# Optimization experiments

Measured on AMD Instinct MI355X. Metric: run time of the kernel, lower is better.

Reference implementation:

```python
import math
import jax, jax.numpy as jnp
import numpy as np

N_HEAD = 8
BLOCK_SIZE = 1024
LN_EPS = 1e-5


def _layer_norm(x, g, b):
    mu = jnp.mean(x, axis=-1, keepdims=True)
    var = jnp.var(x, axis=-1, keepdims=True)
    return (x - mu) * jax.lax.rsqrt(var + LN_EPS) * g + b


def _skew(QEr):
    # QEr: (B, nh, L, L) -> pad one zero column on the left, reshape, drop first row
    B, nh, nr, nc = QEr.shape
    padded = jnp.pad(QEr, ((0, 0), (0, 0), (0, 0), (1, 0)))  # (B, nh, nr, nc+1)
    reshaped = padded.reshape(B, nh, nc + 1, nr)
    return reshaped[:, :, 1:, :]  # (B, nh, nr, nc)


def _attn(x, W_qkv, b_qkv, W_o, b_o, Er):
    B, L, D = x.shape
    hs = D // N_HEAD
    qkv = x @ W_qkv + b_qkv  # (B, L, 3D)
    q, k, v = jnp.split(qkv, 3, axis=-1)
    # (B, nh, L, hs)
    q = q.reshape(B, L, N_HEAD, hs).transpose(0, 2, 1, 3)
    k = k.reshape(B, L, N_HEAD, hs).transpose(0, 2, 1, 3)
    v = v.reshape(B, L, N_HEAD, hs).transpose(0, 2, 1, 3)
    start = BLOCK_SIZE - L
    Er_t = Er[start:, :].T  # (hs, L)
    QEr = q @ Er_t  # (B, nh, L, L)
    Srel = _skew(QEr)
    scores = (jnp.einsum('bhqd,bhkd->bhqk', q, k) + Srel) * (1.0 / math.sqrt(hs))
    causal = jnp.tril(jnp.ones((L, L), dtype=bool))
    scores = jnp.where(causal, scores, jnp.float32(-jnp.inf))
    att = jax.nn.softmax(scores, axis=-1)
    y = jnp.einsum('bhqk,bhkd->bhqd', att, v)
    y = y.transpose(0, 2, 1, 3).reshape(B, L, D)
    return y @ W_o + b_o


def reference(x, W_qkv, b_qkv, W_o, b_o, Er, ln1_g, ln1_b, ln2_g, ln2_b,
              W_fc, b_fc, W_proj, b_proj):
    x = x + _attn(_layer_norm(x, ln1_g, ln1_b), W_qkv, b_qkv, W_o, b_o, Er)
    h = _layer_norm(x, ln2_g, ln2_b) @ W_fc + b_fc
    h = jax.nn.gelu(h, approximate=False)
    h = h @ W_proj + b_proj
    return x + h


def setup_inputs() -> dict:
    key = jax.random.key(0)
    ks = jax.random.split(key, 8)
    B, L, D, F = 8, 1024, 1024, 4096
    hs = D // N_HEAD
    s = lambda fan_in: 1.0 / math.sqrt(fan_in)
    return {
        'x': jax.random.normal(ks[0], (B, L, D), dtype=jnp.float32),
        'W_qkv': jax.random.normal(ks[1], (D, 3 * D), dtype=jnp.float32) * s(D),
        'b_qkv': jnp.zeros((3 * D,), dtype=jnp.float32),
        'W_o': jax.random.normal(ks[2], (D, D), dtype=jnp.float32) * s(D),
        'b_o': jnp.zeros((D,), dtype=jnp.float32),
        'Er': jax.random.normal(ks[3], (BLOCK_SIZE, hs), dtype=jnp.float32),
        'ln1_g': jnp.ones((D,), dtype=jnp.float32),
        'ln1_b': jnp.zeros((D,), dtype=jnp.float32),
        'ln2_g': jnp.ones((D,), dtype=jnp.float32),
        'ln2_b': jnp.zeros((D,), dtype=jnp.float32),
        'W_fc': jax.random.normal(ks[4], (D, F), dtype=jnp.float32) * s(D),
        'b_fc': jnp.zeros((F,), dtype=jnp.float32),
        'W_proj': jax.random.normal(ks[5], (F, D), dtype=jnp.float32) * s(F),
        'b_proj': jnp.zeros((D,), dtype=jnp.float32),
    }
```

## Files before the change

### kernel.cpp

```cpp
#include <hip/hip_runtime.h>
#include <hip/hip_bf16.h>
#include <math.h>

#define BB 8
#define LL 1024
#define DD 1024
#define FF 4096
#define NHH 8
#define HSS 128
#define SCALE 0.08838834764831845f
#define TRI(qi, kt) ((qi) * ((qi) + 1) / 2 + (kt))

typedef __bf16 bf16;
typedef __bf16 bf16x8 __attribute__((ext_vector_type(8)));
typedef float f32x4 __attribute__((ext_vector_type(4)));
typedef _Float16 f16;
typedef _Float16 f16x4 __attribute__((ext_vector_type(4)));

__device__ inline void async_copy16(const void* g, void* l) {
  __builtin_amdgcn_global_load_lds(
      (const __attribute__((address_space(1))) unsigned int*)g,
      (__attribute__((address_space(3))) unsigned int*)l, 16, 0, 0);
}

#define FENCE() asm volatile("" ::: "memory")
#define BARRIER() do { FENCE(); __builtin_amdgcn_s_barrier(); FENCE(); } while (0)
#define VMCNT6() asm volatile("s_waitcnt vmcnt(6)" ::: "memory")

__global__ __launch_bounds__(256)
void transpose_cast_kernel(const float* __restrict__ W, bf16* __restrict__ Wt,
                           int K, int N) {
  __shared__ float tile[32][33];
  int n0 = blockIdx.x * 32, k0 = blockIdx.y * 32;
  int tx = threadIdx.x, ty = threadIdx.y;
#pragma unroll
  for (int i = 0; i < 32; i += 8)
    tile[ty + i][tx] = W[(size_t)(k0 + ty + i) * N + n0 + tx];
  __syncthreads();
#pragma unroll
  for (int i = 0; i < 32; i += 8)
    Wt[(size_t)(n0 + ty + i) * K + k0 + tx] = (bf16)tile[tx][ty + i];
}

__global__ __launch_bounds__(256)
void pack_er_kernel(const float* __restrict__ Er, bf16* __restrict__ ErP) {
  int g = blockIdx.x, tid = threadIdx.x;
  int l15 = tid & 15, quad = (tid >> 4) & 3, st = tid >> 6;
  const float* src = Er + (size_t)(g * 16 + l15) * HSS + st * 32 + quad * 8;
  bf16* dst = ErP + (size_t)g * 2048 + tid * 8;
#pragma unroll
  for (int j = 0; j < 8; j++) dst[j] = (bf16)src[j];
}

__global__ __launch_bounds__(256)
void ln_kernel(const float* __restrict__ x, const float* __restrict__ g,
               const float* __restrict__ bta, bf16* __restrict__ out) {
  int row = blockIdx.x;
  int tid = threadIdx.x;
  const float4 v = ((const float4*)(x + (size_t)row * DD))[tid];
  float s = v.x + v.y + v.z + v.w;
  float s2 = v.x * v.x + v.y * v.y + v.z * v.z + v.w * v.w;
#pragma unroll
  for (int o = 32; o > 0; o >>= 1) {
    s += __shfl_down(s, o);
    s2 += __shfl_down(s2, o);
  }
  __shared__ float a1[4], a2[4];
  int wave = tid >> 6;
  if ((tid & 63) == 0) { a1[wave] = s; a2[wave] = s2; }
  __syncthreads();
  s = a1[0] + a1[1] + a1[2] + a1[3];
  s2 = a2[0] + a2[1] + a2[2] + a2[3];
  float mu = s * (1.0f / DD);
  float rstd = rsqrtf(s2 * (1.0f / DD) - mu * mu + 1e-5f);
  float4 gv = ((const float4*)g)[tid];
  float4 bv = ((const float4*)bta)[tid];
  bf16* o4 = out + (size_t)row * DD + tid * 4;
  o4[0] = (bf16)((v.x - mu) * rstd * gv.x + bv.x);
  o4[1] = (bf16)((v.y - mu) * rstd * gv.y + bv.y);
  o4[2] = (bf16)((v.z - mu) * rstd * gv.z + bv.z);
  o4[3] = (bf16)((v.w - mu) * rstd * gv.w + bv.w);
}

template <int EPI>
__global__ __launch_bounds__(512)
void gemm256_kernel(const bf16* __restrict__ A, const bf16* __restrict__ Bt,
                    const float* __restrict__ bias, void* __restrict__ Cout,
                    int M, int N, int K) {
  __shared__ bf16 Als[2][256 * 64];
  __shared__ bf16 Bls[2][256 * 64];
  int tid = threadIdx.x;
  int wave = tid >> 6, lane = tid & 63;
  int l15 = lane & 15, quad = lane >> 4;
  int wmi = wave >> 2, wni = wave & 3;
  int m0 = blockIdx.y * 256, n0 = blockIdx.x * 256;

  int u0 = tid, u1 = tid + 512;
  int r0 = u0 >> 3, c0 = ((u0 & 7) ^ (r0 & 7)) << 3;
  int r1 = u1 >> 3, c1 = ((u1 & 7) ^ (r1 & 7)) << 3;
  const bf16* aB0 = A + (size_t)(m0 + r0) * K + c0;
  const bf16* aB1 = A + (size_t)(m0 + r1) * K + c1;
  const bf16* bB0 = Bt + (size_t)(n0 + r0) * K + c0;
  const bf16* bB1 = Bt + (size_t)(n0 + r1) * K + c1;
  int d0 = u0 * 8, d1 = u1 * 8;

  auto stageA = [&](int b, int h, int t) {
    size_t off = (size_t)h * 128 * K + (size_t)t * 64;
    async_copy16(aB0 + off, &Als[b][h * 8192 + d0]);
    async_copy16(aB1 + off, &Als[b][h * 8192 + d1]);
  };
  auto stageB = [&](int b, int h, int t) {
    size_t off = (size_t)h * 128 * K + (size_t)t * 64;
    async_copy16(bB0 + off, &Bls[b][h * 8192 + d0]);
    async_copy16(bB1 + off, &Bls[b][h * 8192 + d1]);
  };

  f32x4 acc[8][4] = {};
  bf16x8 af[2][4], bfr[2][2];

  auto readA = [&](int b, int qm) {
#pragma unroll
    for (int kk = 0; kk < 2; kk++)
#pragma unroll
      for (int mt = 0; mt < 4; mt++) {
        int ra = qm * 128 + wmi * 64 + mt * 16 + l15;
        af[kk][mt] = *(const bf16x8*)&Als[b][ra * 64 + (((kk * 4 + quad) ^ (ra & 7)) << 3)];
      }
  };
  auto readB = [&](int b, int qn) {
#pragma unroll
    for (int kk = 0; kk < 2; kk++)
#pragma unroll
      for (int nt = 0; nt < 2; nt++) {
        int rb = qn * 128 + wni * 32 + nt * 16 + l15;
        bfr[kk][nt] = *(const bf16x8*)&Bls[b][rb * 64 + (((kk * 4 + quad) ^ (rb & 7)) << 3)];
      }
  };
  auto mfma16 = [&](int qm, int qn) {
    __builtin_amdgcn_s_setprio(1);
#pragma unroll
    for (int kk = 0; kk < 2; kk++)
#pragma unroll
      for (int mt = 0; mt < 4; mt++)
#pragma unroll
        for (int nt = 0; nt < 2; nt++)
          acc[qm * 4 + mt][qn * 2 + nt] = __builtin_amdgcn_mfma_f32_16x16x32_bf16(
              af[kk][mt], bfr[kk][nt], acc[qm * 4 + mt][qn * 2 + nt], 0, 0, 0);
    __builtin_amdgcn_s_setprio(0);
  };

  int nk = K >> 6;
  stageA(0, 0, 0); stageB(0, 0, 0); stageB(0, 1, 0); stageA(0, 1, 0);
  stageA(1, 0, 1); stageB(1, 1, 1);
  VMCNT6();
  BARRIER();

  for (int t = 0; t < nk; t++) {
    int cur = t & 1;
    readA(cur, 0); readB(cur, 0);
    if (t + 1 < nk) stageB(cur ^ 1, 0, t + 1);
    BARRIER();
    mfma16(0, 0);
    BARRIER();
    readB(cur, 1);
    if (t + 1 < nk) stageA(cur ^ 1, 1, t + 1);
    VMCNT6();
    BARRIER();
    mfma16(0, 1);
    BARRIER();
    readA(cur, 1);
    if (t + 2 < nk) stageA(cur, 0, t + 2);
    BARRIER();
    mfma16(1, 1);
    BARRIER();
    readB(cur, 0);
    if (t + 2 < nk) stageB(cur, 1, t + 2);
    VMCNT6();
    BARRIER();
    mfma16(1, 0);
    BARRIER();
  }

#pragma unroll
  for (int MT = 0; MT < 8; MT++) {
#pragma unroll
    for (int NT = 0; NT < 4; NT++) {
      int col = n0 + (NT >> 1) * 128 + wni * 32 + (NT & 1) * 16 + l15;
      float bv = bias[col];
#pragma unroll
      for (int r = 0; r < 4; r++) {
        int row = m0 + (MT >> 2) * 128 + wmi * 64 + (MT & 3) * 16 + quad * 4 + r;
        float v = acc[MT][NT][r] + bv;
        if (EPI == 1) v = 0.5f * v * (1.0f + erff(v * 0.7071067811865475f));
        ((bf16*)Cout)[(size_t)row * N + col] = (bf16)v;
      }
    }
  }
}

template <int EPI>
__global__ __launch_bounds__(256)
void gemm_kernel(const bf16* __restrict__ A, const bf16* __restrict__ Bt,
                 const float* __restrict__ bias, const float* __restrict__ res,
                 void* __restrict__ Cout, int M, int N, int K) {
  __shared__ bf16 Als[128 * 64];
  __shared__ bf16 Bls[128 * 64];
  int tid = threadIdx.x;
  int wave = tid >> 6, lane = tid & 63;
  int l15 = lane & 15, quad = lane >> 4;

  int m0 = blockIdx.y * 128, n0 = blockIdx.x * 128;
  int wm = (wave >> 1) * 64, wn = (wave & 1) * 64;
  f32x4 acc[4][4] = {};

  const bf16* asrc[4];
  const bf16* bsrc[4];
  int ldso[4];
#pragma unroll
  for (int i = 0; i < 4; i++) {
    int u = i * 256 + tid;
    int row = u >> 3, c = u & 7;
    int g = c ^ (row & 7);
    asrc[i] = A + (size_t)(m0 + row) * K + g * 8;
    bsrc[i] = Bt + (size_t)(n0 + row) * K + g * 8;
    ldso[i] = u * 8;
  }

  for (int k0 = 0; k0 < K; k0 += 64) {
    __syncthreads();
#pragma unroll
    for (int i = 0; i < 4; i++) {
      async_copy16(asrc[i] + k0, &Als[ldso[i]]);
      async_copy16(bsrc[i] + k0, &Bls[ldso[i]]);
    }
    __syncthreads();

    bf16x8 af[2][4], bfr[2][4];
#pragma unroll
    for (int kk = 0; kk < 2; kk++) {
#pragma unroll
      for (int mt = 0; mt < 4; mt++) {
        int ra = wm + mt * 16 + l15;
        af[kk][mt] = *(const bf16x8*)&Als[ra * 64 + (((kk * 4 + quad) ^ (ra & 7)) << 3)];
        int rb = wn + mt * 16 + l15;
        bfr[kk][mt] = *(const bf16x8*)&Bls[rb * 64 + (((kk * 4 + quad) ^ (rb & 7)) << 3)];
      }
    }
#pragma unroll
    for (int kk = 0; kk < 2; kk++)
#pragma unroll
      for (int mt = 0; mt < 4; mt++)
#pragma unroll
        for (int nt = 0; nt < 4; nt++)
          acc[mt][nt] = __builtin_amdgcn_mfma_f32_16x16x32_bf16(af[kk][mt], bfr[kk][nt],
                                                                acc[mt][nt], 0, 0, 0);
  }

#pragma unroll
  for (int mt = 0; mt < 4; mt++) {
#pragma unroll
    for (int nt = 0; nt < 4; nt++) {
      int col = n0 + wn + nt * 16 + l15;
      float bv = bias[col];
#pragma unroll
      for (int r = 0; r < 4; r++) {
        int row = m0 + wm + mt * 16 + quad * 4 + r;
        float v = acc[mt][nt][r] + bv;
        if (EPI == 1) v = 0.5f * v * (1.0f + erff(v * 0.7071067811865475f));
        if (EPI == 2) {
          v += res[(size_t)row * N + col];
          ((float*)Cout)[(size_t)row * N + col] = v;
        } else {
          ((bf16*)Cout)[(size_t)row * N + col] = (bf16)v;
        }
      }
    }
  }
}

__global__ __launch_bounds__(256)
void pack_kv_kernel(const bf16* __restrict__ qkv, bf16* __restrict__ Kpack,
                    bf16* __restrict__ Vpack) {
  __shared__ bf16 Vst[64][132];
  int kt = blockIdx.x, h = blockIdx.y, b = blockIdx.z;
  int tid = threadIdx.x;
  const size_t rs = 3 * DD;
  const bf16* kb = qkv + (size_t)b * LL * rs + (size_t)(kt * 64) * rs + DD + h * HSS;
  const bf16* vb = kb + DD;
  bf16* kp = Kpack + ((size_t)(b * NHH + h) * 16 + kt) * (64 * 128);
  bf16* vp = Vpack + ((size_t)(b * NHH + h) * 16 + kt) * (128 * 64);
#pragma unroll
  for (int i = 0; i < 4; i++) {
    int u = i * 256 + tid;
    int kk = u >> 4, c = u & 15;
    bf16x8 kv = *(const bf16x8*)(kb + (size_t)kk * rs + c * 8);
    *(bf16x8*)(kp + kk * 128 + ((c ^ kk) & 15) * 8) = kv;
    *(bf16x8*)&Vst[kk][c * 8] = *(const bf16x8*)(vb + (size_t)kk * rs + c * 8);
  }
  __syncthreads();
#pragma unroll
  for (int i = 0; i < 4; i++) {
    int u = i * 256 + tid;
    int d = u >> 3, c = u & 7;
    bf16x8 t;
#pragma unroll
    for (int j = 0; j < 8; j++) t[j] = Vst[c * 8 + j][d];
    *(bf16x8*)(vp + d * 64 + ((c ^ (d & 7))) * 8) = t;
  }
}

__global__ __launch_bounds__(256)
void relband_kernel(const bf16* __restrict__ qkv, const bf16* __restrict__ ErP,
                    f16* __restrict__ band) {
  int tid = threadIdx.x, wave = tid >> 6, lane = tid & 63;
  int l15 = lane & 15, quad = lane >> 4;
  int h = blockIdx.y, b = blockIdx.z;
  const size_t rs = 3 * DD;
  const bf16* qbase = qkv + (size_t)b * LL * rs + h * HSS;
  f16* bbase = band + (size_t)(b * NHH + h) * (136 * 4096);

#pragma unroll 1
  for (int ph = 0; ph < 2; ph++) {
    int qb = ph ? 15 - blockIdx.x : blockIdx.x;
    int qw0 = qb * 64 + wave * 16;

    bf16x8 qf[4];
#pragma unroll
    for (int st = 0; st < 4; st++)
      qf[st] = *(const bf16x8*)(qbase + (size_t)(qw0 + l15) * rs + st * 32 + quad * 8);

#pragma unroll 1
    for (int kt = 0; kt <= qb; kt++) {
      int k0 = kt * 64;
      int kmax_off = qw0 + 15 - k0;
      int m_base = 1008 - qw0 + k0;
      int gb = m_base >> 4;
      int ntR = (kmax_off >> 4) + 1;
      if (ntR > 4) ntR = 4;

      f32x4 rr[5] = {};
#pragma unroll
      for (int n = 0; n < 5; n++) {
        if (n <= ntR) {
          int g = gb + n;
          if (g > 63) g = 63;
          const bf16* ep = ErP + (size_t)g * 2048 + lane * 8;
#pragma unroll
          for (int st = 0; st < 4; st++) {
            bf16x8 ef = *(const bf16x8*)(ep + st * 512);
            rr[n] = __builtin_amdgcn_mfma_f32_16x16x32_bf16(qf[st], ef, rr[n], 0, 0, 0);
          }
        }
      }

      f16x4 sf[4];
#pragma unroll
      for (int rg = 0; rg < 4; rg++) {
        int qloc = quad * 4 + rg;
        int tt = 15 - qloc + l15;
        int src = (lane & 48) | (tt & 15);
        float shv[5];
#pragma unroll
        for (int n = 0; n < 5; n++)
          shv[n] = (n <= ntR) ? __shfl(rr[n][rg], src) : 0.f;
#pragma unroll
        for (int nt = 0; nt < 4; nt++)
          sf[nt][rg] = (f16)((tt & 16) ? shv[nt + 1] : shv[nt]);
      }
      f16* tb = bbase + (size_t)TRI(qb, kt) * 4096;
#pragma unroll
      for (int nt = 0; nt < 4; nt++)
        if (nt * 16 <= kmax_off)
          *(f16x4*)(tb + (wave * 4 + nt) * 256 + l15 * 16 + quad * 4) = sf[nt];
    }
  }
}

__global__ __launch_bounds__(256)
void flash_kernel(const bf16* __restrict__ qkv, const bf16* __restrict__ Kpack,
                  const bf16* __restrict__ Vpack, const f16* __restrict__ band,
                  bf16* __restrict__ y) {
  __shared__ bf16 Kls[2][64 * 128];
  __shared__ bf16 Vls[2][128 * 64];
  __shared__ bf16 Pls[4][16][72];

  int tid = threadIdx.x, wave = tid >> 6, lane = tid & 63;
  int l15 = lane & 15, quad = lane >> 4;
  int h = blockIdx.y, b = blockIdx.z;

  const size_t rs = 3 * DD;
  const bf16* qbase = qkv + (size_t)b * LL * rs + h * HSS;
  const bf16* kp = Kpack + (size_t)(b * NHH + h) * 16 * (64 * 128);
  const bf16* vp = Vpack + (size_t)(b * NHH + h) * 16 * (128 * 64);
  const f16* bnd = band + (size_t)(b * NHH + h) * (136 * 4096);

  int buf = 0;
#pragma unroll 1
  for (int ph = 0; ph < 2; ph++) {
    int qb = ph ? 15 - blockIdx.x : blockIdx.x;
    int qw0 = qb * 64 + wave * 16;
    int nkt = qb + 1;

    bf16x8 qf[4];
#pragma unroll
    for (int st = 0; st < 4; st++)
      qf[st] = *(const bf16x8*)(qbase + (size_t)(qw0 + l15) * rs + st * 32 + quad * 8);

    {
      const bf16* ks = kp;
      const bf16* vs = vp;
#pragma unroll
      for (int i = 0; i < 4; i++) {
        int off = (wave * 4 + i) * 512 + lane * 8;
        async_copy16(ks + off, &Kls[buf][off]);
        async_copy16(vs + off, &Vls[buf][off]);
      }
    }

    f32x4 o[8] = {};
    float mrow[4] = {-INFINITY, -INFINITY, -INFINITY, -INFINITY};
    float lrow[4] = {0.f, 0.f, 0.f, 0.f};

#pragma unroll 1
    for (int kt = 0; kt < nkt; kt++) {
      int k0 = kt * 64;
      int kmax_off = qw0 + 15 - k0;
      __syncthreads();

      const f16* tb = bnd + (size_t)TRI(qb, kt) * 4096;
      f16x4 srl[4] = {};
#pragma unroll
      for (int nt = 0; nt < 4; nt++)
        if (nt * 16 <= kmax_off)
          srl[nt] = *(const f16x4*)(tb + (wave * 4 + nt) * 256 + l15 * 16 + quad * 4);

      if (kt + 1 < nkt) {
        const bf16* ks = kp + (size_t)(kt + 1) * (64 * 128);
        const bf16* vs = vp + (size_t)(kt + 1) * (128 * 64);
#pragma unroll
        for (int i = 0; i < 4; i++) {
          int off = (wave * 4 + i) * 512 + lane * 8;
          async_copy16(ks + off, &Kls[buf ^ 1][off]);
          async_copy16(vs + off, &Vls[buf ^ 1][off]);
        }
      }

      f32x4 sa[4] = {};
#pragma unroll
      for (int nt = 0; nt < 4; nt++) {
        if (nt * 16 <= kmax_off) {
          int kk = nt * 16 + l15;
#pragma unroll
          for (int st = 0; st < 4; st++) {
            bf16x8 kf = *(const bf16x8*)&Kls[buf][kk * 128 + (((st * 4 + quad) ^ l15) & 15) * 8];
            sa[nt] = __builtin_amdgcn_mfma_f32_16x16x32_bf16(qf[st], kf, sa[nt], 0, 0, 0);
          }
        }
      }

      float pmx[4] = {-INFINITY, -INFINITY, -INFINITY, -INFINITY};
#pragma unroll
      for (int nt = 0; nt < 4; nt++) {
        if (nt * 16 <= kmax_off) {
          int kg = k0 + nt * 16 + l15;
#pragma unroll
          for (int rg = 0; rg < 4; rg++) {
            int qg = qw0 + quad * 4 + rg;
            float v = (sa[nt][rg] + (float)srl[nt][rg]) * SCALE;
            v = (kg <= qg) ? v : -INFINITY;
            sa[nt][rg] = v;
            pmx[rg] = fmaxf(pmx[rg], v);
          }
        } else {
#pragma unroll
          for (int rg = 0; rg < 4; rg++) sa[nt][rg] = -INFINITY;
        }
      }

#pragma unroll
      for (int rg = 0; rg < 4; rg++) {
        float v = pmx[rg];
        v = fmaxf(v, __shfl_xor(v, 1));
        v = fmaxf(v, __shfl_xor(v, 2));
        v = fmaxf(v, __shfl_xor(v, 4));
        v = fmaxf(v, __shfl_xor(v, 8));
        float mnew = fmaxf(mrow[rg], v);
        float alpha = __expf(mrow[rg] - mnew);
        mrow[rg] = mnew;
        lrow[rg] *= alpha;
#pragma unroll
        for (int nt = 0; nt < 8; nt++) o[nt][rg] *= alpha;
        pmx[rg] = mnew;
      }
      float ls[4] = {0.f, 0.f, 0.f, 0.f};
#pragma unroll
      for (int nt = 0; nt < 4; nt++)
#pragma unroll
        for (int rg = 0; rg < 4; rg++) {
          float p = __expf(sa[nt][rg] - pmx[rg]);
          ls[rg] += p;
          Pls[wave][quad * 4 + rg][nt * 16 + l15] = (bf16)p;
        }
#pragma unroll
      for (int rg = 0; rg < 4; rg++) {
        float v = ls[rg];
        v += __shfl_xor(v, 1);
        v += __shfl_xor(v, 2);
        v += __shfl_xor(v, 4);
        v += __shfl_xor(v, 8);
        lrow[rg] += v;
      }

      bf16x8 pf[2];
#pragma unroll
      for (int s2 = 0; s2 < 2; s2++)
        pf[s2] = *(const bf16x8*)&Pls[wave][l15][s2 * 32 + quad * 8];
#pragma unroll
      for (int nt = 0; nt < 8; nt++) {
        int d = nt * 16 + l15;
#pragma unroll
        for (int s2 = 0; s2 < 2; s2++) {
          if (s2 * 32 <= kmax_off) {
            bf16x8 vf = *(const bf16x8*)&Vls[buf][d * 64 + (((s2 * 4 + quad) ^ (l15 & 7)) & 7) * 8];
            o[nt] = __builtin_amdgcn_mfma_f32_16x16x32_bf16(pf[s2], vf, o[nt], 0, 0, 0);
          }
        }
      }
      buf ^= 1;
    }

#pragma unroll
    for (int rg = 0; rg < 4; rg++) {
      float inv = 1.0f / lrow[rg];
      int qg = qw0 + quad * 4 + rg;
      bf16* yr = y + ((size_t)b * LL + qg) * DD + h * HSS;
#pragma unroll
      for (int nt = 0; nt < 8; nt++) yr[nt * 16 + l15] = (bf16)(o[nt][rg] * inv);
    }
  }
}

extern "C" void kernel_launch(void* const* d_in, const int* in_sizes, int n_in,
                              void* d_out, int out_size, void* d_ws, size_t ws_size,
                              hipStream_t stream) {
  const float* x = (const float*)d_in[0];
  const float* W_qkv = (const float*)d_in[1];
  const float* b_qkv = (const float*)d_in[2];
  const float* W_o = (const float*)d_in[3];
  const float* b_o = (const float*)d_in[4];
  const float* Er = (const float*)d_in[5];
  const float* ln1_g = (const float*)d_in[6];
  const float* ln1_b = (const float*)d_in[7];
  const float* ln2_g = (const float*)d_in[8];
  const float* ln2_b = (const float*)d_in[9];
  const float* W_fc = (const float*)d_in[10];
  const float* b_fc = (const float*)d_in[11];
  const float* W_proj = (const float*)d_in[12];
  const float* b_proj = (const float*)d_in[13];
  float* out = (float*)d_out;

  char* p = (char*)d_ws;
  auto alloc = [&](size_t bytes) {
    char* r = p;
    p += (bytes + 255) & ~(size_t)255;
    return r;
  };
  bf16* Wt_qkv = (bf16*)alloc((size_t)3072 * 1024 * 2);
  bf16* Wt_o   = (bf16*)alloc((size_t)1024 * 1024 * 2);
  bf16* Wt_fc  = (bf16*)alloc((size_t)4096 * 1024 * 2);
  bf16* Wt_pr  = (bf16*)alloc((size_t)1024 * 4096 * 2);
  bf16* ErP    = (bf16*)alloc((size_t)1024 * 128 * 2);
  bf16* xn     = (bf16*)alloc((size_t)8192 * 1024 * 2);
  bf16* qkvb   = (bf16*)alloc((size_t)8192 * 3072 * 2);
  bf16* yb     = (bf16*)alloc((size_t)8192 * 1024 * 2);
  bf16* Kpack  = (bf16*)alloc((size_t)64 * 16 * 64 * 128 * 2);
  bf16* Vpack  = (bf16*)alloc((size_t)64 * 16 * 128 * 64 * 2);
  f16*  band   = (f16*)alloc((size_t)64 * 136 * 4096 * 2);
  float* x2    = (float*)band;
  bf16* hb     = qkvb;

  transpose_cast_kernel<<<dim3(3072 / 32, 1024 / 32), dim3(32, 8), 0, stream>>>(W_qkv, Wt_qkv, 1024, 3072);
  transpose_cast_kernel<<<dim3(1024 / 32, 1024 / 32), dim3(32, 8), 0, stream>>>(W_o, Wt_o, 1024, 1024);
  transpose_cast_kernel<<<dim3(4096 / 32, 1024 / 32), dim3(32, 8), 0, stream>>>(W_fc, Wt_fc, 1024, 4096);
  transpose_cast_kernel<<<dim3(1024 / 32, 4096 / 32), dim3(32, 8), 0, stream>>>(W_proj, Wt_pr, 4096, 1024);
  pack_er_kernel<<<64, 256, 0, stream>>>(Er, ErP);

  ln_kernel<<<8192, 256, 0, stream>>>(x, ln1_g, ln1_b, xn);
  gemm256_kernel<0><<<dim3(12, 32), 512, 0, stream>>>(xn, Wt_qkv, b_qkv, qkvb, 8192, 3072, 1024);
  pack_kv_kernel<<<dim3(16, 8, 8), 256, 0, stream>>>(qkvb, Kpack, Vpack);
  relband_kernel<<<dim3(8, 8, 8), 256, 0, stream>>>(qkvb, ErP, band);
  flash_kernel<<<dim3(8, 8, 8), 256, 0, stream>>>(qkvb, Kpack, Vpack, band, yb);
  gemm_kernel<2><<<dim3(8, 64), 256, 0, stream>>>(yb, Wt_o, b_o, x, x2, 8192, 1024, 1024);
  ln_kernel<<<8192, 256, 0, stream>>>(x2, ln2_g, ln2_b, xn);
  gemm256_kernel<1><<<dim3(16, 32), 512, 0, stream>>>(xn, Wt_fc, b_fc, hb, 8192, 4096, 1024);
  gemm_kernel<2><<<dim3(8, 64), 256, 0, stream>>>(hb, Wt_pr, b_proj, x2, out, 8192, 1024, 4096);
}
```

Before: 600.3 us.

## Add 256x128 GEMM kernel for QKV and proj; unroll 256x256 GEMM loop

Adds a new 256x128-tile, 512-thread GEMM kernel with a double-buffered B tile and finer vmcnt waits. It is used for the QKV projection and for the final MLP projection with residual, replacing the 256x256 kernel and the 128x128 kernel respectively. The existing 256x256 kernel's k-loop is unrolled by two with constant buffer indices, and both B halves are read up front into separate registers. The smaller tile raises the block count for QKV to improve CU occupancy and wave balance, at the cost of lower per-block reuse and more registers in the unrolled loop.

```diff
diff --git a/kernel.cpp b/kernel.cpp
--- a/kernel.cpp
+++ b/kernel.cpp
@@ -25,6 +25,9 @@
 
 #define FENCE() asm volatile("" ::: "memory")
 #define BARRIER() do { FENCE(); __builtin_amdgcn_s_barrier(); FENCE(); } while (0)
+#define VMCNT0() asm volatile("s_waitcnt vmcnt(0)" ::: "memory")
+#define VMCNT2() asm volatile("s_waitcnt vmcnt(2)" ::: "memory")
+#define VMCNT4() asm volatile("s_waitcnt vmcnt(4)" ::: "memory")
 #define VMCNT6() asm volatile("s_waitcnt vmcnt(6)" ::: "memory")
 
 __global__ __launch_bounds__(256)
@@ -116,7 +119,7 @@
   };
 
   f32x4 acc[8][4] = {};
-  bf16x8 af[2][4], bfr[2][2];
+  bf16x8 af[2][4], bfr[2][2][2];
 
   auto readA = [&](int b, int qm) {
 #pragma unroll
@@ -133,7 +136,7 @@
 #pragma unroll
       for (int nt = 0; nt < 2; nt++) {
         int rb = qn * 128 + wni * 32 + nt * 16 + l15;
-        bfr[kk][nt] = *(const bf16x8*)&Bls[b][rb * 64 + (((kk * 4 + quad) ^ (rb & 7)) << 3)];
+        bfr[qn][kk][nt] = *(const bf16x8*)&Bls[b][rb * 64 + (((kk * 4 + quad) ^ (rb & 7)) << 3)];
       }
   };
   auto mfma16 = [&](int qm, int qn) {
@@ -145,7 +148,7 @@
 #pragma unroll
         for (int nt = 0; nt < 2; nt++)
           acc[qm * 4 + mt][qn * 2 + nt] = __builtin_amdgcn_mfma_f32_16x16x32_bf16(
-              af[kk][mt], bfr[kk][nt], acc[qm * 4 + mt][qn * 2 + nt], 0, 0, 0);
+              af[kk][mt], bfr[qn][kk][nt], acc[qm * 4 + mt][qn * 2 + nt], 0, 0, 0);
     __builtin_amdgcn_s_setprio(0);
   };
 
@@ -155,30 +158,32 @@
   VMCNT6();
   BARRIER();
 
-  for (int t = 0; t < nk; t++) {
-    int cur = t & 1;
-    readA(cur, 0); readB(cur, 0);
-    if (t + 1 < nk) stageB(cur ^ 1, 0, t + 1);
-    BARRIER();
-    mfma16(0, 0);
-    BARRIER();
-    readB(cur, 1);
-    if (t + 1 < nk) stageA(cur ^ 1, 1, t + 1);
-    VMCNT6();
-    BARRIER();
-    mfma16(0, 1);
-    BARRIER();
-    readA(cur, 1);
-    if (t + 2 < nk) stageA(cur, 0, t + 2);
-    BARRIER();
-    mfma16(1, 1);
-    BARRIER();
-    readB(cur, 0);
-    if (t + 2 < nk) stageB(cur, 1, t + 2);
-    VMCNT6();
-    BARRIER();
-    mfma16(1, 0);
-    BARRIER();
+  for (int t = 0; t < nk; t += 2) {
+#pragma unroll
+    for (int uu = 0; uu < 2; uu++) {
+      const int tt = t + uu;
+      const int cur = uu;
+      readA(cur, 0); readB(cur, 0); readB(cur, 1);
+      if (tt + 1 < nk) stageB(cur ^ 1, 0, tt + 1);
+      BARRIER();
+      mfma16(0, 0);
+      BARRIER();
+      if (tt + 1 < nk) stageA(cur ^ 1, 1, tt + 1);
+      VMCNT6();
+      BARRIER();
+      mfma16(0, 1);
+      BARRIER();
+      readA(cur, 1);
+      if (tt + 2 < nk) stageA(cur, 0, tt + 2);
+      BARRIER();
+      mfma16(1, 1);
+      BARRIER();
+      if (tt + 2 < nk) stageB(cur, 1, tt + 2);
+      VMCNT6();
+      BARRIER();
+      mfma16(1, 0);
+      BARRIER();
+    }
   }
 
 #pragma unroll
@@ -193,6 +198,120 @@
         float v = acc[MT][NT][r] + bv;
         if (EPI == 1) v = 0.5f * v * (1.0f + erff(v * 0.7071067811865475f));
         ((bf16*)Cout)[(size_t)row * N + col] = (bf16)v;
+      }
+    }
+  }
+}
+
+template <int EPI>
+__global__ __launch_bounds__(512)
+void gemm256n_kernel(const bf16* __restrict__ A, const bf16* __restrict__ Bt,
+                     const float* __restrict__ bias, const float* __restrict__ res,
+                     void* __restrict__ Cout, int M, int N, int K) {
+  __shared__ bf16 Als[2][256 * 64];
+  __shared__ bf16 Bls[2][128 * 64];
+  int tid = threadIdx.x;
+  int wave = tid >> 6, lane = tid & 63;
+  int l15 = lane & 15, quad = lane >> 4;
+  int wmi = wave >> 2, wni = wave & 3;
+  int m0 = blockIdx.y * 256, n0 = blockIdx.x * 128;
+
+  int u0 = tid, u1 = tid + 512;
+  int r0 = u0 >> 3, c0 = ((u0 & 7) ^ (r0 & 7)) << 3;
+  int r1 = u1 >> 3, c1 = ((u1 & 7) ^ (r1 & 7)) << 3;
+  const bf16* aB0 = A + (size_t)(m0 + r0) * K + c0;
+  const bf16* aB1 = A + (size_t)(m0 + r1) * K + c1;
+  const bf16* bB0 = Bt + (size_t)(n0 + r0) * K + c0;
+  const bf16* bB1 = Bt + (size_t)(n0 + r1) * K + c1;
+  int d0 = u0 * 8, d1 = u1 * 8;
+
+  auto stageA = [&](int b, int h, int t) {
+    size_t off = (size_t)h * 128 * K + (size_t)t * 64;
+    async_copy16(aB0 + off, &Als[b][h * 8192 + d0]);
+    async_copy16(aB1 + off, &Als[b][h * 8192 + d1]);
+  };
+  auto stageB = [&](int b, int t) {
+    size_t off = (size_t)t * 64;
+    async_copy16(bB0 + off, &Bls[b][d0]);
+    async_copy16(bB1 + off, &Bls[b][d1]);
+  };
+
+  f32x4 acc[8][2] = {};
+  bf16x8 af[2][4], bfr[2][2];
+
+  auto readA = [&](int b, int qm) {
+#pragma unroll
+    for (int kk = 0; kk < 2; kk++)
+#pragma unroll
+      for (int mt = 0; mt < 4; mt++) {
+        int ra = qm * 128 + wmi * 64 + mt * 16 + l15;
+        af[kk][mt] = *(const bf16x8*)&Als[b][ra * 64 + (((kk * 4 + quad) ^ (ra & 7)) << 3)];
+      }
+  };
+  auto readB = [&](int b) {
+#pragma unroll
+    for (int kk = 0; kk < 2; kk++)
+#pragma unroll
+      for (int nt = 0; nt < 2; nt++) {
+        int rb = wni * 32 + nt * 16 + l15;
+        bfr[kk][nt] = *(const bf16x8*)&Bls[b][rb * 64 + (((kk * 4 + quad) ^ (rb & 7)) << 3)];
+      }
+  };
+  auto mfma16 = [&](int qm) {
+    __builtin_amdgcn_s_setprio(1);
+#pragma unroll
+    for (int kk = 0; kk < 2; kk++)
+#pragma unroll
+      for (int mt = 0; mt < 4; mt++)
+#pragma unroll
+        for (int nt = 0; nt < 2; nt++)
+          acc[qm * 4 + mt][nt] = __builtin_amdgcn_mfma_f32_16x16x32_bf16(
+              af[kk][mt], bfr[kk][nt], acc[qm * 4 + mt][nt], 0, 0, 0);
+    __builtin_amdgcn_s_setprio(0);
+  };
+
+  int nk = K >> 6;
+  stageB(0, 0); stageB(1, 1); stageA(0, 0, 0); stageA(0, 1, 0);
+  VMCNT0();
+  BARRIER();
+
+  for (int t = 0; t < nk; t += 2) {
+#pragma unroll
+    for (int uu = 0; uu < 2; uu++) {
+      const int tt = t + uu;
+      const int cur = uu;
+      readA(cur, 0); readB(cur);
+      if (tt + 1 < nk) { stageA(cur ^ 1, 0, tt + 1); VMCNT4(); }
+      else { VMCNT0(); }
+      BARRIER();
+      mfma16(0);
+      BARRIER();
+      readA(cur, 1);
+      if (tt + 1 < nk) stageA(cur ^ 1, 1, tt + 1);
+      if (tt + 2 < nk) { stageB(cur, tt + 2); VMCNT4(); }
+      else { VMCNT2(); }
+      BARRIER();
+      mfma16(1);
+      BARRIER();
+    }
+  }
+
+#pragma unroll
+  for (int MT = 0; MT < 8; MT++) {
+#pragma unroll
+    for (int NT = 0; NT < 2; NT++) {
+      int col = n0 + wni * 32 + NT * 16 + l15;
+      float bv = bias[col];
+#pragma unroll
+      for (int r = 0; r < 4; r++) {
+        int row = m0 + (MT >> 2) * 128 + wmi * 64 + (MT & 3) * 16 + quad * 4 + r;
+        float v = acc[MT][NT][r] + bv;
+        if (EPI == 2) {
+          v += res[(size_t)row * N + col];
+          ((float*)Cout)[(size_t)row * N + col] = v;
+        } else {
+          ((bf16*)Cout)[(size_t)row * N + col] = (bf16)v;
+        }
       }
     }
   }
@@ -586,12 +705,12 @@
   pack_er_kernel<<<64, 256, 0, stream>>>(Er, ErP);
 
   ln_kernel<<<8192, 256, 0, stream>>>(x, ln1_g, ln1_b, xn);
-  gemm256_kernel<0><<<dim3(12, 32), 512, 0, stream>>>(xn, Wt_qkv, b_qkv, qkvb, 8192, 3072, 1024);
+  gemm256n_kernel<0><<<dim3(24, 32), 512, 0, stream>>>(xn, Wt_qkv, b_qkv, nullptr, qkvb, 8192, 3072, 1024);
   pack_kv_kernel<<<dim3(16, 8, 8), 256, 0, stream>>>(qkvb, Kpack, Vpack);
   relband_kernel<<<dim3(8, 8, 8), 256, 0, stream>>>(qkvb, ErP, band);
   flash_kernel<<<dim3(8, 8, 8), 256, 0, stream>>>(qkvb, Kpack, Vpack, band, yb);
   gemm_kernel<2><<<dim3(8, 64), 256, 0, stream>>>(yb, Wt_o, b_o, x, x2, 8192, 1024, 1024);
   ln_kernel<<<8192, 256, 0, stream>>>(x2, ln2_g, ln2_b, xn);
   gemm256_kernel<1><<<dim3(16, 32), 512, 0, stream>>>(xn, Wt_fc, b_fc, hb, 8192, 4096, 1024);
-  gemm_kernel<2><<<dim3(8, 64), 256, 0, stream>>>(hb, Wt_pr, b_proj, x2, out, 8192, 1024, 4096);
-}
+  gemm256n_kernel<2><<<dim3(8, 32), 512, 0, stream>>>(hb, Wt_pr, b_proj, x2, out, 8192, 1024, 4096);
+}
```

Result: no change. 591.8 us (-1.4%).
